# Kernel tuning notes

Hardware: AMD Instinct MI355X
Metric: run time of the kernel (lower is better)

The kernel has to match this reference:

```python
import jax, jax.numpy as jnp
from jax import lax
import numpy as np

B, C, H, W, OUTC, KS = 4, 64, 128, 128, 64, 3
N = KS * KS
PAD = 1
STRIDE = 1


def conv2d(x, w, b, stride, pad):
    out = lax.conv_general_dilated(x, w, (stride, stride), ((pad, pad), (pad, pad)),
                                   dimension_numbers=('NCHW', 'OIHW', 'NCHW'))
    if b is not None:
        out = out + b[None, :, None, None]
    return out


def setup_inputs() -> dict:
    key = jax.random.key(0)
    k = jax.random.split(key, 8)
    f = jnp.float32

    def w_init(kk, shape, fan_in, scale=1.0):
        return jax.random.normal(kk, shape, f) * (scale / np.sqrt(fan_in))

    return {
        'x': jax.random.normal(k[0], (B, C, H, W), f),
        'ref': jax.random.normal(k[1], (B, C, H, W), f),
        'w_cd': w_init(k[2], (C, 2 * C, 1, 1), 2 * C),
        'b_cd': jnp.zeros((C,), f),
        'w_p': w_init(k[3], (2 * N, C, 3, 3), C * 9, 0.1),  # small offsets, keeps sampling stable
        'b_p': jnp.zeros((2 * N,), f),
        'w_m': w_init(k[4], (N, C, 3, 3), C * 9),
        'b_m': jnp.zeros((N,), f),
        'w_c': w_init(k[5], (N * C, C, 3, 3), C * 9),
        'b_c': jnp.zeros((N * C,), f),
        'w_conv': w_init(k[6], (OUTC, C, KS, KS), C * KS * KS),
    }


def deform_forward(x, ref, w_cd, b_cd, w_p, b_p, w_m, b_m, w_c, b_c, w_conv):
    b, c, h, w = x.shape
    fused = conv2d(jnp.concatenate([x, ref], axis=1), w_cd, b_cd, 1, 0)
    offset = conv2d(fused, w_p, b_p, STRIDE, 1)             # [b, 2N, h, w]
    m = jax.nn.sigmoid(conv2d(fused, w_m, b_m, STRIDE, 1))  # [b, N, h, w]
    c_off = jnp.tanh(conv2d(fused, w_c, b_c, STRIDE, 1))    # [b, N*c, h, w]

    xp = jnp.pad(x, ((0, 0), (0, 0), (PAD, PAD), (PAD, PAD)))
    Hp, Wp = h + 2 * PAD, w + 2 * PAD

    # kernel-relative grid p_n (first N entries = rows, last N = cols)
    r = jnp.arange(-(KS - 1) // 2, (KS - 1) // 2 + 1)
    pnx, pny = jnp.meshgrid(r, r, indexing='ij')
    p_n = jnp.concatenate([pnx.ravel(), pny.ravel()]).reshape(1, 2 * N, 1, 1)
    # base grid p_0 starts at 1 because of the zero padding
    gx, gy = jnp.meshgrid(jnp.arange(1, h * STRIDE + 1, STRIDE),
                          jnp.arange(1, w * STRIDE + 1, STRIDE), indexing='ij')
    p_0 = jnp.concatenate([jnp.broadcast_to(gx[None, None], (1, N, h, w)),
                           jnp.broadcast_to(gy[None, None], (1, N, h, w))], axis=1)
    p = (p_0 + p_n).astype(offset.dtype) + offset           # [b, 2N, h, w]
    p = p.transpose(0, 2, 3, 1)                             # [b, h, w, 2N]

    q_lt = jnp.floor(lax.stop_gradient(p))
    q_rb = q_lt + 1

    def clampq(q):
        return jnp.concatenate([jnp.clip(q[..., :N], 0, Hp - 1),
                                jnp.clip(q[..., N:], 0, Wp - 1)], axis=-1).astype(jnp.int32)

    q_lt = clampq(q_lt)
    q_rb = clampq(q_rb)
    q_lb = jnp.concatenate([q_lt[..., :N], q_rb[..., N:]], axis=-1)
    q_rt = jnp.concatenate([q_rb[..., :N], q_lt[..., N:]], axis=-1)
    p = jnp.concatenate([jnp.clip(p[..., :N], 0, Hp - 1),
                         jnp.clip(p[..., N:], 0, Wp - 1)], axis=-1)

    def gweight(q, sx, sy):
        qx = q[..., :N].astype(p.dtype)
        qy = q[..., N:].astype(p.dtype)
        return (1 + sx * (qx - p[..., :N])) * (1 + sy * (qy - p[..., N:]))

    g_lt = gweight(q_lt, 1, 1)
    g_rb = gweight(q_rb, -1, -1)
    g_lb = gweight(q_lb, 1, -1)
    g_rt = gweight(q_rt, -1, 1)

    x_flat = xp.reshape(b, c, Hp * Wp)

    def get_x_q(q):
        idx = q[..., :N] * Wp + q[..., N:]                  # [b, h, w, N]
        xq = jnp.take_along_axis(x_flat, idx.reshape(b, 1, -1), axis=2)
        return xq.reshape(b, c, h, w, N)

    x_off = (g_lt[:, None] * get_x_q(q_lt) + g_rb[:, None] * get_x_q(q_rb)
             + g_lb[:, None] * get_x_q(q_lb) + g_rt[:, None] * get_x_q(q_rt))

    # color deformation: [b, N*c, h, w] -> [b, c, h, w, N]
    x_off = x_off + c_off.reshape(b, c, N, h, w).transpose(0, 1, 3, 4, 2)
    # modulation broadcast over channels
    x_off = x_off * m.transpose(0, 2, 3, 1)[:, None]

    # [b,c,h,w,N] -> [b,c,h*ks,w*ks] with N = (kernel_row, kernel_col)
    x_off = x_off.reshape(b, c, h, w, KS, KS).transpose(0, 1, 2, 4, 3, 5)
    x_off = x_off.reshape(b, c, h * KS, w * KS)
    return conv2d(x_off, w_conv, None, KS, 0)


def reference(x, ref, w_cd, b_cd, w_p, b_p, w_m, b_m, w_c, b_c, w_conv):
    return deform_forward(x, ref, w_cd, b_cd, w_p, b_p, w_m, b_m, w_c, b_c, w_conv)
```

## Files before the change

### kernel.cpp

```cpp
#include <hip/hip_runtime.h>
#include <hip/hip_fp16.h>


typedef __attribute__((ext_vector_type(8))) __bf16 bf16x8;
typedef __attribute__((ext_vector_type(16))) float f32x16;
#define MFMA32(a, b, c) __builtin_amdgcn_mfma_f32_32x32x16_bf16((a), (b), (c), 0, 0, 0)

#define WS_AC    0
#define WS_APM   368640
#define WS_ACONV 387072
#define WS_WCD   428032
#define WS_F2    436224

struct f2pair { float x, y; };

__device__ __forceinline__ unsigned short f2bf(float f) {
    unsigned u = __float_as_uint(f);
    return (unsigned short)((u + 0x7FFFu + ((u >> 16) & 1u)) >> 16);
}
__device__ __forceinline__ float fast_rcp(float x) {
#if __has_builtin(__builtin_amdgcn_rcpf)
    return __builtin_amdgcn_rcpf(x);
#else
    return 1.0f / x;
#endif
}
__device__ __forceinline__ float fast_tanh(float x) {
    float t = __expf(2.0f * x);
    return 1.0f - 2.0f * fast_rcp(t + 1.0f);
}
__device__ __forceinline__ float fast_sigmoid(float x) {
    return fast_rcp(1.0f + __expf(-x));
}

__global__ void prep_kernel(const float* __restrict__ w_c, const float* __restrict__ w_p,
                            const float* __restrict__ w_m, const float* __restrict__ w_conv,
                            const float* __restrict__ w_cd, unsigned short* __restrict__ ws) {
    int i = blockIdx.x * 256 + threadIdx.x;
    if (i >= 436224) return;
    float val;
    if (i < WS_APM) {
        int t = i, j = t & 7, l = (t >> 3) & 63, r = t >> 9, ks = r % 36, gmt = r / 36;
        int row = gmt * 32 + (l & 31);
        int kp = ks * 16 + (l >> 5) * 8 + j, tap = kp >> 6, ci = kp & 63;
        val = (row < 576) ? w_c[row * 576 + ci * 9 + tap] : 0.0f;
    } else if (i < WS_ACONV) {
        int t = i - WS_APM, j = t & 7, l = (t >> 3) & 63, ks = t >> 9;
        int row = l & 31;
        int kp = ks * 16 + (l >> 5) * 8 + j, tap = kp >> 6, ci = kp & 63;
        val = (row < 18) ? w_p[row * 576 + ci * 9 + tap]
            : (row < 27) ? w_m[(row - 18) * 576 + ci * 9 + tap] : 0.0f;
    } else if (i < WS_WCD) {
        int t = i - WS_ACONV, j = t & 7, l = (t >> 3) & 63, r = t >> 9;
        int gks = r % 40, ocT = r / 40;
        int oc = ocT * 32 + (l & 31);
        int krow = gks * 16 + (l >> 5) * 8 + j;
        val = (krow < 576) ? w_conv[oc * 576 + krow] : 0.0f;
    } else {
        val = w_cd[i - WS_WCD];
    }
    ws[i] = f2bf(val);
}

__device__ __forceinline__ uint4 stage_load64(const unsigned short* f2b, int h,
                                              int px0, int chunk, int tid) {
    int tap = chunk >> 1;
    int dh = tap / 3 - 1, dw = tap % 3 - 1;
    int hs = h + dh;
    int kg = tid >> 6, px = tid & 63;
    int cg = (chunk & 1) * 4 + kg;
    int wsrc = px0 + px + dw;
    uint4 pk = {0u, 0u, 0u, 0u};
    if (((unsigned)hs < 128u) && ((unsigned)wsrc < 128u))
        pk = *(const uint4*)(f2b + (((size_t)cg << 14) + (hs << 7) + wsrc) * 8);
    return pk;
}
__device__ __forceinline__ void stage_write64(char* Bst, uint4 pk, int tid) {
    int kg = tid >> 6, px = tid & 63;
    *(uint4*)(Bst + ((kg >> 1) * 2 + (px >> 5)) * 1024
                  + ((px & 31) + 32 * (kg & 1)) * 16) = pk;
}

__global__ __launch_bounds__(256, 4)
void k2_fused(const float* __restrict__ x, const float* __restrict__ ref,
              const float* __restrict__ b_cd, const unsigned short* __restrict__ wsbf,
              unsigned short* __restrict__ ws) {
    __shared__ __align__(16) char B0[32768];
    const int tid = threadIdx.x, l = tid & 63, w = tid >> 6;
    const int b = blockIdx.y, p0 = blockIdx.x * 128;
    const int rl31 = l & 31, kh8 = (l >> 5) * 8;

    #pragma unroll
    for (int it = 0; it < 8; ++it) {
        int task = it * 256 + tid;
        int kg = task >> 7, px = task & 127;
        const float* src = (kg < 8) ? x : ref;
        int kbase = (kg & 7) * 8;
        unsigned short v[8];
        #pragma unroll
        for (int j = 0; j < 8; ++j)
            v[j] = f2bf(src[(((size_t)b * 64 + kbase + j) << 14) + p0 + px]);
        uint4 pk;
        pk.x = (unsigned)v[0] | ((unsigned)v[1] << 16);
        pk.y = (unsigned)v[2] | ((unsigned)v[3] << 16);
        pk.z = (unsigned)v[4] | ((unsigned)v[5] << 16);
        pk.w = (unsigned)v[6] | ((unsigned)v[7] << 16);
        *(uint4*)(B0 + ((kg >> 1) * 4 + (px >> 5)) * 1024
                      + ((px & 31) + 32 * (kg & 1)) * 16) = pk;
    }
    __syncthreads();

    f32x16 a0, a1;
    #pragma unroll
    for (int r = 0; r < 16; ++r) { a0[r] = 0.0f; a1[r] = 0.0f; }
    const unsigned short* A0 = wsbf + WS_WCD + rl31 * 128 + kh8;
    #pragma unroll
    for (int s = 0; s < 8; ++s) {
        bf16x8 bf = *(bf16x8*)(B0 + ((s * 4 + w) * 64 + l) * 16);
        bf16x8 x0 = *(const bf16x8*)(A0 + s * 16);
        bf16x8 x1 = *(const bf16x8*)(A0 + 32 * 128 + s * 16);
        a0 = MFMA32(x0, bf, a0);
        a1 = MFMA32(x1, bf, a1);
    }
    unsigned short* f2 = ws + WS_F2 + ((size_t)b << 20);
    int px = p0 + w * 32 + rl31;
    int h4 = (l >> 5) * 4;
    #pragma unroll
    for (int t = 0; t < 2; ++t)
        #pragma unroll
        for (int q = 0; q < 4; ++q) {
            ushort4 st;
            float v0 = (t ? a1[q * 4 + 0] : a0[q * 4 + 0]) + b_cd[t * 32 + 8 * q + h4 + 0];
            float v1 = (t ? a1[q * 4 + 1] : a0[q * 4 + 1]) + b_cd[t * 32 + 8 * q + h4 + 1];
            float v2 = (t ? a1[q * 4 + 2] : a0[q * 4 + 2]) + b_cd[t * 32 + 8 * q + h4 + 2];
            float v3 = (t ? a1[q * 4 + 3] : a0[q * 4 + 3]) + b_cd[t * 32 + 8 * q + h4 + 3];
            st.x = f2bf(v0); st.y = f2bf(v1); st.z = f2bf(v2); st.w = f2bf(v3);
            *(ushort4*)(f2 + ((size_t)((t * 4 + q) << 14) + px) * 8 + h4) = st;
        }
}

__global__ __launch_bounds__(256, 4)
void k3_main(const float* __restrict__ x, const float* __restrict__ b_c,
             const float* __restrict__ b_p, const float* __restrict__ b_m,
             const unsigned short* __restrict__ wsbf, float* __restrict__ out) {
    __shared__ __align__(16) char lds[27904];
    char* R = lds;
    float* uL = (float*)lds;
    short* sidx = (short*)(lds + 16384);
    unsigned short* w4h = (unsigned short*)(lds + 18688);
    float* mL = (float*)(lds + 23296);
    float* bcL = (float*)(lds + 25600);

    const int tid = threadIdx.x, l = tid & 63, w = tid >> 6;
    const int id = blockIdx.x;
    const int hbLin = (id & 7) * 128 + (id >> 3);
    const int half = hbLin & 1, b = (hbLin >> 1) & 3, h = hbLin >> 3;
    const int px0 = half * 64;
    const unsigned short* f2b = wsbf + WS_F2 + ((size_t)b << 20);

    for (int i = tid; i < 576; i += 256) bcL[i] = b_c[i];

    {
        f32x16 pm;
        #pragma unroll
        for (int r = 0; r < 16; ++r) pm[r] = 0.0f;
        uint4 a0 = stage_load64(f2b, h, px0, 0, tid);
        uint4 a1 = stage_load64(f2b, h, px0, 1, tid);
        stage_write64(R, a0, tid);
        stage_write64(R + 4096, a1, tid);
        uint4 b0 = stage_load64(f2b, h, px0, 2, tid);
        uint4 b1 = stage_load64(f2b, h, px0, 3, tid);
        __syncthreads();
        #pragma unroll 1
        for (int it = 0; it < 9; ++it) {
            char* cur = R + (it & 1) * 8192;
            char* nxt = R + ((it + 1) & 1) * 8192;
            uint4 c0 = b0, c1 = b1;
            if (it < 7) {
                c0 = stage_load64(f2b, h, px0, 2 * it + 4, tid);
                c1 = stage_load64(f2b, h, px0, 2 * it + 5, tid);
            }
            if (w < 2) {
                #pragma unroll
                for (int q = 0; q < 4; ++q) {
                    int ks = it * 4 + q;
                    bf16x8 bf = *(bf16x8*)(cur + (q >> 1) * 4096
                                               + (((q & 1) * 2 + w) * 64 + l) * 16);
                    bf16x8 apm = *(const bf16x8*)(wsbf + WS_APM + ((ks * 64 + l) << 3));
                    pm = MFMA32(apm, bf, pm);
                }
            }
            if (it < 8) {
                stage_write64(nxt, b0, tid);
                stage_write64(nxt + 4096, b1, tid);
            }
            __syncthreads();
            b0 = c0; b1 = c1;
        }
        if (w < 2) {
            int pxp = w * 32 + (l & 31);
            #pragma unroll
            for (int reg = 0; reg < 16; ++reg) {
                int rl = (reg & 3) + 8 * (reg >> 2) + 4 * (l >> 5);
                uL[rl * 64 + pxp] = pm[reg];
            }
        }
        __syncthreads();
    }

    #pragma unroll 1
    for (int i = tid; i < 576; i += 256) {
        int n = i >> 6, px = i & 63;
        float offr = uL[n * 64 + px] + b_p[n];
        float offc = uL[(9 + n) * 64 + px] + b_p[9 + n];
        float mraw = uL[(18 + n) * 64 + px] + b_m[n];
        int nr = n / 3, nc = n - nr * 3;
        float pr = (float)(h + nr) + offr;
        float pc = (float)(px0 + px + nc) + offc;
        float flr = floorf(pr), flc = floorf(pc);
        float prc = fminf(fmaxf(pr, 0.0f), 129.0f);
        float pcc = fminf(fmaxf(pc, 0.0f), 129.0f);
        float q0r = fminf(fmaxf(flr, 0.0f), 129.0f);
        float q1r = fminf(fmaxf(flr + 1.0f, 0.0f), 129.0f);
        int ir0 = (int)q0r, ir1 = (int)q1r;
        bool vr0 = (ir0 >= 1) && (ir0 <= 128), vr1 = (ir1 >= 1) && (ir1 <= 128);
        float wr0 = vr0 ? (1.0f + q0r - prc) : 0.0f;
        float wr1 = vr1 ? (1.0f - (q1r - prc)) : 0.0f;
        float q0c = fminf(fmaxf(flc, 0.0f), 129.0f);
        float q1c = fminf(fmaxf(flc + 1.0f, 0.0f), 129.0f);
        int ic0 = (int)q0c, ic1 = (int)q1c;
        bool vc0 = (ic0 >= 1) && (ic0 <= 128), vc1 = (ic1 >= 1) && (ic1 <= 128);
        float wc0 = vc0 ? (1.0f + q0c - pcc) : 0.0f;
        float wc1 = vc1 ? (1.0f - (q1c - pcc)) : 0.0f;
        int cx0 = ic0 - 1, cx1 = ic1 - 1;
        int base = min(max(cx0, 0), 126);
        float ws0 = ((base == cx0) && vc0 ? wc0 : 0.0f)
                  + ((base == cx1) && vc1 ? wc1 : 0.0f);
        float ws1 = ((base + 1 == cx0) && vc0 ? wc0 : 0.0f)
                  + ((base + 1 == cx1) && vc1 ? wc1 : 0.0f);
        int rx0 = min(max(ir0 - 1, 0), 127), rx1 = min(max(ir1 - 1, 0), 127);
        short2 s2;
        s2.x = (short)(rx0 * 128 + base);
        s2.y = (short)(rx1 * 128 + base);
        ((short2*)sidx)[px * 9 + n] = s2;
        int wb = (px * 9 + n) * 4;
        w4h[wb + 0] = __half_as_ushort(__float2half(wr0 * ws0));
        w4h[wb + 1] = __half_as_ushort(__float2half(wr0 * ws1));
        w4h[wb + 2] = __half_as_ushort(__float2half(wr1 * ws0));
        w4h[wb + 3] = __half_as_ushort(__float2half(wr1 * ws1));
        mL[n * 64 + px] = fast_sigmoid(mraw);
    }

    f32x16 oa;
    #pragma unroll
    for (int r = 0; r < 16; ++r) oa[r] = 0.0f;
    const float* xb = x + (((size_t)b * 64) << 14);
    const int ocT = w >> 1, nT2 = w & 1;

    #pragma unroll 1
    for (int p = 0; p < 5; ++p) {
        const int mt = p * 4 + w;
        f32x16 acc[2];
        #pragma unroll
        for (int j = 0; j < 2; ++j)
            #pragma unroll
            for (int r = 0; r < 16; ++r) acc[j][r] = 0.0f;

        uint4 a0 = stage_load64(f2b, h, px0, 0, tid);
        uint4 a1 = stage_load64(f2b, h, px0, 1, tid);
        uint4 b0 = stage_load64(f2b, h, px0, 2, tid);
        uint4 b1 = stage_load64(f2b, h, px0, 3, tid);
        __syncthreads();
        stage_write64(R, a0, tid);
        stage_write64(R + 4096, a1, tid);
        __syncthreads();

        #pragma unroll 1
        for (int it = 0; it < 9; ++it) {
            char* cur = R + (it & 1) * 8192;
            char* nxt = R + ((it + 1) & 1) * 8192;
            uint4 c0 = b0, c1 = b1;
            if (it < 7) {
                c0 = stage_load64(f2b, h, px0, 2 * it + 4, tid);
                c1 = stage_load64(f2b, h, px0, 2 * it + 5, tid);
            }
            #pragma unroll
            for (int q = 0; q < 4; ++q) {
                const int ks = it * 4 + q;
                char* fb = cur + (q >> 1) * 4096;
                bf16x8 bf0 = *(bf16x8*)(fb + (((q & 1) * 2 + 0) * 64 + l) * 16);
                bf16x8 bf1 = *(bf16x8*)(fb + (((q & 1) * 2 + 1) * 64 + l) * 16);
                bf16x8 af = *(const bf16x8*)(wsbf + WS_AC
                                + (((mt * 36 + ks) * 64 + l) << 3));
                acc[0] = MFMA32(af, bf0, acc[0]);
                acc[1] = MFMA32(af, bf1, acc[1]);
            }
            if (it < 8) {
                stage_write64(nxt, b0, tid);
                stage_write64(nxt + 4096, b1, tid);
            }
            __syncthreads();
            b0 = c0; b1 = c1;
        }

        const int rowbase = mt * 32;
        #pragma unroll
        for (int j = 0; j < 2; ++j) {
            const int pxe = j * 32 + (l & 31);
            if (rowbase < 576) {
                #pragma unroll
                for (int reg = 0; reg < 16; ++reg) {
                    int rl = (reg & 3) + 8 * (reg >> 2) + 4 * (l >> 5);
                    int row = rowbase + rl;
                    int c = row / 9, n = row - c * 9;
                    float uv = acc[j][reg] + bcL[row];
                    float t = fast_tanh(uv);
                    short2 s2 = ((short2*)sidx)[pxe * 9 + n];
                    int wb = (pxe * 9 + n) * 4;
                    uint2 wv = *(const uint2*)(w4h + wb);
                    float w0 = __half2float(__ushort_as_half((unsigned short)(wv.x & 0xffffu)));
                    float w1 = __half2float(__ushort_as_half((unsigned short)(wv.x >> 16)));
                    float w2 = __half2float(__ushort_as_half((unsigned short)(wv.y & 0xffffu)));
                    float w3 = __half2float(__ushort_as_half((unsigned short)(wv.y >> 16)));
                    const float* xp = xb + ((size_t)c << 14);
                    f2pair v0 = *(const f2pair*)(xp + s2.x);
                    f2pair v1 = *(const f2pair*)(xp + s2.y);
                    float samp = w0 * v0.x + w1 * v0.y + w2 * v1.x + w3 * v1.y;
                    acc[j][reg] = mL[n * 64 + pxe] * (samp + t);
                    if ((reg & 3) == 3) __builtin_amdgcn_sched_barrier(0);
                }
            } else {
                #pragma unroll
                for (int reg = 0; reg < 16; ++reg) acc[j][reg] = 0.0f;
            }
        }

        #pragma unroll
        for (int j = 0; j < 2; ++j) {
            #pragma unroll
            for (int reg = 0; reg < 16; ++reg) {
                int rl = (reg & 3) + 8 * (reg >> 2) + 4 * (l >> 5);
                int k = w * 32 + rl;
                *(unsigned short*)(R + ((k >> 4) * 2 + j) * 1024
                        + ((l & 31) + 32 * ((k >> 3) & 1)) * 16 + (k & 7) * 2)
                    = f2bf(acc[j][reg]);
            }
        }
        __syncthreads();
        #pragma unroll
        for (int ks8 = 0; ks8 < 8; ++ks8) {
            bf16x8 af = *(const bf16x8*)(wsbf + WS_ACONV
                            + (((ocT * 40 + p * 8 + ks8) * 64 + l) << 3));
            bf16x8 bf = *(bf16x8*)(R + (ks8 * 2 + nT2) * 1024 + l * 16);
            oa = MFMA32(af, bf, oa);
        }
    }

    float* ob = out + (((size_t)b * 64) << 14) + (h << 7) + px0 + nT2 * 32 + (l & 31);
    #pragma unroll
    for (int reg = 0; reg < 16; ++reg) {
        int rl = (reg & 3) + 8 * (reg >> 2) + 4 * (l >> 5);
        int oc = ocT * 32 + rl;
        ob[(size_t)oc << 14] = oa[reg];
    }
}

extern "C" void kernel_launch(void* const* d_in, const int* in_sizes, int n_in,
                              void* d_out, int out_size, void* d_ws, size_t ws_size,
                              hipStream_t stream) {
    const float* x      = (const float*)d_in[0];
    const float* ref    = (const float*)d_in[1];
    const float* w_cd   = (const float*)d_in[2];
    const float* b_cd   = (const float*)d_in[3];
    const float* w_p    = (const float*)d_in[4];
    const float* b_p    = (const float*)d_in[5];
    const float* w_m    = (const float*)d_in[6];
    const float* b_m    = (const float*)d_in[7];
    const float* w_c    = (const float*)d_in[8];
    const float* b_c    = (const float*)d_in[9];
    const float* w_conv = (const float*)d_in[10];
    float* out = (float*)d_out;
    unsigned short* wsbf = (unsigned short*)d_ws;

    hipLaunchKernelGGL(prep_kernel, dim3(1704), dim3(256), 0, stream,
                       w_c, w_p, w_m, w_conv, w_cd, wsbf);
    hipLaunchKernelGGL(k2_fused, dim3(128, 4), dim3(256), 0, stream,
                       x, ref, b_cd, wsbf, wsbf);
    hipLaunchKernelGGL(k3_main, dim3(1024), dim3(256), 0, stream,
                       x, b_c, b_p, b_m, wsbf, out);
}
```

Baseline: 224.5 us.

## Load conv B operands directly from global and fuse offset conv into first pass

```diff
diff --git a/kernel.cpp b/kernel.cpp
--- a/kernel.cpp
+++ b/kernel.cpp
@@ -62,23 +62,12 @@
     ws[i] = f2bf(val);
 }
 
-__device__ __forceinline__ uint4 stage_load64(const unsigned short* f2b, int h,
-                                              int px0, int chunk, int tid) {
-    int tap = chunk >> 1;
-    int dh = tap / 3 - 1, dw = tap % 3 - 1;
-    int hs = h + dh;
-    int kg = tid >> 6, px = tid & 63;
-    int cg = (chunk & 1) * 4 + kg;
-    int wsrc = px0 + px + dw;
+__device__ __forceinline__ uint4 loadB4(const unsigned short* f2b, int hs,
+                                        int wsrc, int cg) {
     uint4 pk = {0u, 0u, 0u, 0u};
     if (((unsigned)hs < 128u) && ((unsigned)wsrc < 128u))
         pk = *(const uint4*)(f2b + (((size_t)cg << 14) + (hs << 7) + wsrc) * 8);
     return pk;
-}
-__device__ __forceinline__ void stage_write64(char* Bst, uint4 pk, int tid) {
-    int kg = tid >> 6, px = tid & 63;
-    *(uint4*)(Bst + ((kg >> 1) * 2 + (px >> 5)) * 1024
-                  + ((px & 31) + 32 * (kg & 1)) * 16) = pk;
 }
 
 __global__ __launch_bounds__(256, 4)
@@ -152,6 +141,7 @@
     float* bcL = (float*)(lds + 25600);
 
     const int tid = threadIdx.x, l = tid & 63, w = tid >> 6;
+    const int lh = l >> 5, l31 = l & 31;
     const int id = blockIdx.x;
     const int hbLin = (id & 7) * 128 + (id >> 3);
     const int half = hbLin & 1, b = (hbLin >> 1) & 3, h = hbLin >> 3;
@@ -160,97 +150,6 @@
 
     for (int i = tid; i < 576; i += 256) bcL[i] = b_c[i];
 
-    {
-        f32x16 pm;
-        #pragma unroll
-        for (int r = 0; r < 16; ++r) pm[r] = 0.0f;
-        uint4 a0 = stage_load64(f2b, h, px0, 0, tid);
-        uint4 a1 = stage_load64(f2b, h, px0, 1, tid);
-        stage_write64(R, a0, tid);
-        stage_write64(R + 4096, a1, tid);
-        uint4 b0 = stage_load64(f2b, h, px0, 2, tid);
-        uint4 b1 = stage_load64(f2b, h, px0, 3, tid);
-        __syncthreads();
-        #pragma unroll 1
-        for (int it = 0; it < 9; ++it) {
-            char* cur = R + (it & 1) * 8192;
-            char* nxt = R + ((it + 1) & 1) * 8192;
-            uint4 c0 = b0, c1 = b1;
-            if (it < 7) {
-                c0 = stage_load64(f2b, h, px0, 2 * it + 4, tid);
-                c1 = stage_load64(f2b, h, px0, 2 * it + 5, tid);
-            }
-            if (w < 2) {
-                #pragma unroll
-                for (int q = 0; q < 4; ++q) {
-                    int ks = it * 4 + q;
-                    bf16x8 bf = *(bf16x8*)(cur + (q >> 1) * 4096
-                                               + (((q & 1) * 2 + w) * 64 + l) * 16);
-                    bf16x8 apm = *(const bf16x8*)(wsbf + WS_APM + ((ks * 64 + l) << 3));
-                    pm = MFMA32(apm, bf, pm);
-                }
-            }
-            if (it < 8) {
-                stage_write64(nxt, b0, tid);
-                stage_write64(nxt + 4096, b1, tid);
-            }
-            __syncthreads();
-            b0 = c0; b1 = c1;
-        }
-        if (w < 2) {
-            int pxp = w * 32 + (l & 31);
-            #pragma unroll
-            for (int reg = 0; reg < 16; ++reg) {
-                int rl = (reg & 3) + 8 * (reg >> 2) + 4 * (l >> 5);
-                uL[rl * 64 + pxp] = pm[reg];
-            }
-        }
-        __syncthreads();
-    }
-
-    #pragma unroll 1
-    for (int i = tid; i < 576; i += 256) {
-        int n = i >> 6, px = i & 63;
-        float offr = uL[n * 64 + px] + b_p[n];
-        float offc = uL[(9 + n) * 64 + px] + b_p[9 + n];
-        float mraw = uL[(18 + n) * 64 + px] + b_m[n];
-        int nr = n / 3, nc = n - nr * 3;
-        float pr = (float)(h + nr) + offr;
-        float pc = (float)(px0 + px + nc) + offc;
-        float flr = floorf(pr), flc = floorf(pc);
-        float prc = fminf(fmaxf(pr, 0.0f), 129.0f);
-        float pcc = fminf(fmaxf(pc, 0.0f), 129.0f);
-        float q0r = fminf(fmaxf(flr, 0.0f), 129.0f);
-        float q1r = fminf(fmaxf(flr + 1.0f, 0.0f), 129.0f);
-        int ir0 = (int)q0r, ir1 = (int)q1r;
-        bool vr0 = (ir0 >= 1) && (ir0 <= 128), vr1 = (ir1 >= 1) && (ir1 <= 128);
-        float wr0 = vr0 ? (1.0f + q0r - prc) : 0.0f;
-        float wr1 = vr1 ? (1.0f - (q1r - prc)) : 0.0f;
-        float q0c = fminf(fmaxf(flc, 0.0f), 129.0f);
-        float q1c = fminf(fmaxf(flc + 1.0f, 0.0f), 129.0f);
-        int ic0 = (int)q0c, ic1 = (int)q1c;
-        bool vc0 = (ic0 >= 1) && (ic0 <= 128), vc1 = (ic1 >= 1) && (ic1 <= 128);
-        float wc0 = vc0 ? (1.0f + q0c - pcc) : 0.0f;
-        float wc1 = vc1 ? (1.0f - (q1c - pcc)) : 0.0f;
-        int cx0 = ic0 - 1, cx1 = ic1 - 1;
-        int base = min(max(cx0, 0), 126);
-        float ws0 = ((base == cx0) && vc0 ? wc0 : 0.0f)
-                  + ((base == cx1) && vc1 ? wc1 : 0.0f);
-        float ws1 = ((base + 1 == cx0) && vc0 ? wc0 : 0.0f)
-                  + ((base + 1 == cx1) && vc1 ? wc1 : 0.0f);
-        int rx0 = min(max(ir0 - 1, 0), 127), rx1 = min(max(ir1 - 1, 0), 127);
-        short2 s2;
-        s2.x = (short)(rx0 * 128 + base);
-        s2.y = (short)(rx1 * 128 + base);
-        ((short2*)sidx)[px * 9 + n] = s2;
-        int wb = (px * 9 + n) * 4;
-        w4h[wb + 0] = __half_as_ushort(__float2half(wr0 * ws0));
-        w4h[wb + 1] = __half_as_ushort(__float2half(wr0 * ws1));
-        w4h[wb + 2] = __half_as_ushort(__float2half(wr1 * ws0));
-        w4h[wb + 3] = __half_as_ushort(__float2half(wr1 * ws1));
-        mL[n * 64 + px] = fast_sigmoid(mraw);
-    }
-
     f32x16 oa;
     #pragma unroll
     for (int r = 0; r < 16; ++r) oa[r] = 0.0f;
@@ -260,60 +159,97 @@
     #pragma unroll 1
     for (int p = 0; p < 5; ++p) {
         const int mt = p * 4 + w;
-        f32x16 acc[2];
+        const bool dopm = (p == 0) && (w < 2);
+        f32x16 acc0, acc1, pm;
         #pragma unroll
-        for (int j = 0; j < 2; ++j)
-            #pragma unroll
-            for (int r = 0; r < 16; ++r) acc[j][r] = 0.0f;
-
-        uint4 a0 = stage_load64(f2b, h, px0, 0, tid);
-        uint4 a1 = stage_load64(f2b, h, px0, 1, tid);
-        uint4 b0 = stage_load64(f2b, h, px0, 2, tid);
-        uint4 b1 = stage_load64(f2b, h, px0, 3, tid);
-        __syncthreads();
-        stage_write64(R, a0, tid);
-        stage_write64(R + 4096, a1, tid);
-        __syncthreads();
-
-        #pragma unroll 1
-        for (int it = 0; it < 9; ++it) {
-            char* cur = R + (it & 1) * 8192;
-            char* nxt = R + ((it + 1) & 1) * 8192;
-            uint4 c0 = b0, c1 = b1;
-            if (it < 7) {
-                c0 = stage_load64(f2b, h, px0, 2 * it + 4, tid);
-                c1 = stage_load64(f2b, h, px0, 2 * it + 5, tid);
-            }
-            #pragma unroll
-            for (int q = 0; q < 4; ++q) {
-                const int ks = it * 4 + q;
-                char* fb = cur + (q >> 1) * 4096;
-                bf16x8 bf0 = *(bf16x8*)(fb + (((q & 1) * 2 + 0) * 64 + l) * 16);
-                bf16x8 bf1 = *(bf16x8*)(fb + (((q & 1) * 2 + 1) * 64 + l) * 16);
-                bf16x8 af = *(const bf16x8*)(wsbf + WS_AC
-                                + (((mt * 36 + ks) * 64 + l) << 3));
-                acc[0] = MFMA32(af, bf0, acc[0]);
-                acc[1] = MFMA32(af, bf1, acc[1]);
-            }
-            if (it < 8) {
-                stage_write64(nxt, b0, tid);
-                stage_write64(nxt + 4096, b1, tid);
+        for (int r = 0; r < 16; ++r) { acc0[r] = 0.0f; acc1[r] = 0.0f; pm[r] = 0.0f; }
+
+        const unsigned short* Abase = wsbf + WS_AC + (((size_t)mt * 36) * 64 + l) * 8;
+        #pragma unroll 4
+        for (int ks = 0; ks < 36; ++ks) {
+            int tap = ks >> 2;
+            int dh = tap / 3 - 1, dw = tap % 3 - 1;
+            int hs = h + dh;
+            int cg = ((ks & 3) << 1) + lh;
+            int w0c = px0 + l31 + dw;
+            uint4 pk0 = loadB4(f2b, hs, w0c, cg);
+            uint4 pk1 = loadB4(f2b, hs, w0c + 32, cg);
+            bf16x8 bf0 = *(bf16x8*)&pk0;
+            bf16x8 bf1 = *(bf16x8*)&pk1;
+            bf16x8 af = *(const bf16x8*)(Abase + (size_t)ks * 512);
+            acc0 = MFMA32(af, bf0, acc0);
+            acc1 = MFMA32(af, bf1, acc1);
+            if (dopm) {
+                bf16x8 apm = *(const bf16x8*)(wsbf + WS_APM + ((ks * 64 + l) << 3));
+                pm = MFMA32(apm, w ? bf1 : bf0, pm);
+            }
+        }
+
+        if (p == 0) {
+            if (w < 2) {
+                int pxp = w * 32 + l31;
+                #pragma unroll
+                for (int reg = 0; reg < 16; ++reg) {
+                    int rl = (reg & 3) + 8 * (reg >> 2) + 4 * lh;
+                    uL[rl * 64 + pxp] = pm[reg];
+                }
             }
             __syncthreads();
-            b0 = c0; b1 = c1;
+            #pragma unroll 1
+            for (int i = tid; i < 576; i += 256) {
+                int n = i >> 6, px = i & 63;
+                float offr = uL[n * 64 + px] + b_p[n];
+                float offc = uL[(9 + n) * 64 + px] + b_p[9 + n];
+                float mraw = uL[(18 + n) * 64 + px] + b_m[n];
+                int nr = n / 3, nc = n - nr * 3;
+                float pr = (float)(h + nr) + offr;
+                float pc = (float)(px0 + px + nc) + offc;
+                float flr = floorf(pr), flc = floorf(pc);
+                float prc = fminf(fmaxf(pr, 0.0f), 129.0f);
+                float pcc = fminf(fmaxf(pc, 0.0f), 129.0f);
+                float q0r = fminf(fmaxf(flr, 0.0f), 129.0f);
+                float q1r = fminf(fmaxf(flr + 1.0f, 0.0f), 129.0f);
+                int ir0 = (int)q0r, ir1 = (int)q1r;
+                bool vr0 = (ir0 >= 1) && (ir0 <= 128), vr1 = (ir1 >= 1) && (ir1 <= 128);
+                float wr0 = vr0 ? (1.0f + q0r - prc) : 0.0f;
+                float wr1 = vr1 ? (1.0f - (q1r - prc)) : 0.0f;
+                float q0c = fminf(fmaxf(flc, 0.0f), 129.0f);
+                float q1c = fminf(fmaxf(flc + 1.0f, 0.0f), 129.0f);
+                int ic0 = (int)q0c, ic1 = (int)q1c;
+                bool vc0 = (ic0 >= 1) && (ic0 <= 128), vc1 = (ic1 >= 1) && (ic1 <= 128);
+                float wc0 = vc0 ? (1.0f + q0c - pcc) : 0.0f;
+                float wc1 = vc1 ? (1.0f - (q1c - pcc)) : 0.0f;
+                int cx0 = ic0 - 1, cx1 = ic1 - 1;
+                int base = min(max(cx0, 0), 126);
+                float ws0 = ((base == cx0) && vc0 ? wc0 : 0.0f)
+                          + ((base == cx1) && vc1 ? wc1 : 0.0f);
+                float ws1 = ((base + 1 == cx0) && vc0 ? wc0 : 0.0f)
+                          + ((base + 1 == cx1) && vc1 ? wc1 : 0.0f);
+                int rx0 = min(max(ir0 - 1, 0), 127), rx1 = min(max(ir1 - 1, 0), 127);
+                short2 s2;
+                s2.x = (short)(rx0 * 128 + base);
+                s2.y = (short)(rx1 * 128 + base);
+                ((short2*)sidx)[px * 9 + n] = s2;
+                int wb = (px * 9 + n) * 4;
+                w4h[wb + 0] = __half_as_ushort(__float2half(wr0 * ws0));
+                w4h[wb + 1] = __half_as_ushort(__float2half(wr0 * ws1));
+                w4h[wb + 2] = __half_as_ushort(__float2half(wr1 * ws0));
+                w4h[wb + 3] = __half_as_ushort(__float2half(wr1 * ws1));
+                mL[n * 64 + px] = fast_sigmoid(mraw);
+            }
+            __syncthreads();
         }
 
         const int rowbase = mt * 32;
-        #pragma unroll
-        for (int j = 0; j < 2; ++j) {
-            const int pxe = j * 32 + (l & 31);
+        auto epi = [&](f32x16& a, int j) {
+            const int pxe = j * 32 + l31;
             if (rowbase < 576) {
                 #pragma unroll
                 for (int reg = 0; reg < 16; ++reg) {
-                    int rl = (reg & 3) + 8 * (reg >> 2) + 4 * (l >> 5);
+                    int rl = (reg & 3) + 8 * (reg >> 2) + 4 * lh;
                     int row = rowbase + rl;
                     int c = row / 9, n = row - c * 9;
-                    float uv = acc[j][reg] + bcL[row];
+                    float uv = a[reg] + bcL[row];
                     float t = fast_tanh(uv);
                     short2 s2 = ((short2*)sidx)[pxe * 9 + n];
                     int wb = (pxe * 9 + n) * 4;
@@ -326,26 +262,30 @@
                     f2pair v0 = *(const f2pair*)(xp + s2.x);
                     f2pair v1 = *(const f2pair*)(xp + s2.y);
                     float samp = w0 * v0.x + w1 * v0.y + w2 * v1.x + w3 * v1.y;
-                    acc[j][reg] = mL[n * 64 + pxe] * (samp + t);
+                    a[reg] = mL[n * 64 + pxe] * (samp + t);
                     if ((reg & 3) == 3) __builtin_amdgcn_sched_barrier(0);
                 }
             } else {
                 #pragma unroll
-                for (int reg = 0; reg < 16; ++reg) acc[j][reg] = 0.0f;
-            }
-        }
-
-        #pragma unroll
-        for (int j = 0; j < 2; ++j) {
+                for (int reg = 0; reg < 16; ++reg) a[reg] = 0.0f;
+            }
+        };
+        epi(acc0, 0);
+        epi(acc1, 1);
+
+        if (p > 0) __syncthreads();
+        auto scat = [&](const f32x16& a, int j) {
             #pragma unroll
             for (int reg = 0; reg < 16; ++reg) {
-                int rl = (reg & 3) + 8 * (reg >> 2) + 4 * (l >> 5);
+                int rl = (reg & 3) + 8 * (reg >> 2) + 4 * lh;
                 int k = w * 32 + rl;
                 *(unsigned short*)(R + ((k >> 4) * 2 + j) * 1024
-                        + ((l & 31) + 32 * ((k >> 3) & 1)) * 16 + (k & 7) * 2)
-                    = f2bf(acc[j][reg]);
-            }
-        }
+                        + (l31 + 32 * ((k >> 3) & 1)) * 16 + (k & 7) * 2)
+                    = f2bf(a[reg]);
+            }
+        };
+        scat(acc0, 0);
+        scat(acc1, 1);
         __syncthreads();
         #pragma unroll
         for (int ks8 = 0; ks8 < 8; ++ks8) {
@@ -356,10 +296,10 @@
         }
     }
 
-    float* ob = out + (((size_t)b * 64) << 14) + (h << 7) + px0 + nT2 * 32 + (l & 31);
+    float* ob = out + (((size_t)b * 64) << 14) + (h << 7) + px0 + nT2 * 32 + l31;
     #pragma unroll
     for (int reg = 0; reg < 16; ++reg) {
-        int rl = (reg & 3) + 8 * (reg >> 2) + 4 * (l >> 5);
+        int rl = (reg & 3) + 8 * (reg >> 2) + 4 * lh;
         int oc = ocT * 32 + rl;
         ob[(size_t)oc << 14] = oa[reg];
     }
```

Result: slower. 247.9 us (+10.4%).
